# Optimization experiments

Hardware: AMD Instinct MI355X
Metric: run time of the kernel (lower is better)

The kernel has to match this reference:

```python
import jax, jax.numpy as jnp
import numpy as np

B, T, D, H, G = 32, 1000, 512, 512, 8
LN_EPS = 1e-5


def setup_inputs() -> dict:
    key = jax.random.key(0)
    ks = jax.random.split(key, 6)
    return {
        "x": jax.random.normal(ks[0], (B, T, D), jnp.float32),
        "w_in": jax.random.normal(ks[1], (G, D // G, H // G), jnp.float32) * 0.05,
        "w_rec_W": jax.random.normal(ks[2], (2 * H, H), jnp.float32) * 0.05,
        "u_rec": jax.random.normal(ks[3], (2 * H, H), jnp.float32) * 0.05,
        "ln_gamma": jnp.ones((2 * H,), jnp.float32),
        "ln_beta": jnp.zeros((2 * H,), jnp.float32),
        "w_out": jax.random.normal(ks[4], (G, H // G, D // G), jnp.float32) * 0.05,
    }


def grouped_linear(x, w):
    # x: [B,T,G*I], w: [G,I,Ho] -> [B,T,G*Ho]
    b, t, _ = x.shape
    g, i, ho = w.shape
    y = jnp.einsum('btgi,gih->btgh', x.reshape(b, t, g, i), w)
    return y.reshape(b, t, g * ho)


def layernorm(w, gamma, beta):
    mu = jnp.mean(w, axis=-1, keepdims=True)
    var = jnp.var(w, axis=-1, keepdims=True)
    return (w - mu) * jax.lax.rsqrt(var + LN_EPS) * gamma + beta


def ligru_scan(w, u):
    # w: [B,T,2H] precomputed input projection; u: [2H,H] recurrent weight
    ut = u.T  # [H, 2H]
    h0 = jnp.zeros((w.shape[0], u.shape[1]), w.dtype)

    def step(h, wt):
        gates = wt + h @ ut            # [B, 2H]
        at, zt = jnp.split(gates, 2, axis=1)
        zt = jax.nn.sigmoid(zt)
        hcand = jax.nn.relu(at)        # drop_mask = 1.0 (eval)
        h = zt * h + (1.0 - zt) * hcand
        return h, h

    _, hs = jax.lax.scan(step, h0, jnp.swapaxes(w, 0, 1))  # [T,B,H]
    return jnp.swapaxes(hs, 0, 1)  # [B,T,H]


def reference(x, w_in, w_rec_W, u_rec, ln_gamma, ln_beta, w_out):
    h_in = grouped_linear(x, w_in)              # [B,T,H]
    w = jnp.einsum('bth,gh->btg', h_in, w_rec_W)  # [B,T,2H]
    w = layernorm(w, ln_gamma, ln_beta)
    h = ligru_scan(w, u_rec)                    # [B,T,H]
    return grouped_linear(h, w_out)             # [B,T,D]
```

## Files before the change

### kernel.cpp

```cpp
#include <hip/hip_runtime.h>
#include <cstddef>

#define B_SZ 32
#define T_LEN 1000
#define LN_EPS 1e-5f

typedef short bf16x8 __attribute__((ext_vector_type(8)));
typedef float f32x4 __attribute__((ext_vector_type(4)));

__device__ __forceinline__ unsigned short f2bf(float f) {
    unsigned u = __builtin_bit_cast(unsigned, f);
    u += 0x7FFFu + ((u >> 16) & 1u);
    return (unsigned short)(u >> 16);
}

__global__ __launch_bounds__(256) void kw(const float* __restrict__ w_rec,
                                          unsigned short* __restrict__ wrt) {
    int idx  = blockIdx.x * 256 + threadIdx.x;
    int lane = idx & 63;
    int nt   = (idx >> 6) & 63;
    int kt   = idx >> 12;
    int n    = nt * 16 + (lane & 15);
    int k0   = kt * 32 + (lane >> 4) * 8;
    const float* src = w_rec + (size_t)n * 512 + k0;
    unsigned short* dst = wrt + (size_t)idx * 8;
#pragma unroll
    for (int j = 0; j < 8; ++j) dst[j] = f2bf(src[j]);
}

__global__ __launch_bounds__(256) void k1(const float* __restrict__ x,
                                          const float* __restrict__ w_in,
                                          unsigned short* __restrict__ hin) {
    __shared__ alignas(16) float xt[16][512];
    const int tid  = threadIdx.x;
    const int row0 = blockIdx.x * 16;

    for (int i = tid; i < 16 * 128; i += 256) {
        int rr = i >> 7, c4 = i & 127;
        ((float4*)xt[rr])[c4] =
            ((const float4*)(x + (size_t)(row0 + rr) * 512))[c4];
    }
    __syncthreads();

    for (int q = 0; q < 2; ++q) {
        const int c = tid + (q << 8);
        const int g = c >> 6, o = c & 63;
        const float* wb = w_in + (g << 12) + o;
        float wcol[64];
#pragma unroll
        for (int ii = 0; ii < 64; ++ii) wcol[ii] = wb[ii << 6];
#pragma unroll 4
        for (int rr = 0; rr < 16; ++rr) {
            float acc = 0.f;
#pragma unroll
            for (int ii = 0; ii < 64; ++ii) acc += xt[rr][(g << 6) + ii] * wcol[ii];
            hin[(size_t)(row0 + rr) * 512 + c] = f2bf(acc);
        }
    }
}

#define ALD 536
__global__ __launch_bounds__(256) void k2(const unsigned short* __restrict__ hin,
                                          const unsigned short* __restrict__ wrt,
                                          const float* __restrict__ gamma,
                                          const float* __restrict__ beta,
                                          float* __restrict__ w_pre) {
    __shared__ alignas(16) unsigned short At[32 * ALD];
    __shared__ float redS[4][32];
    __shared__ float redQ[4][32];
    __shared__ float stat[2][32];

    const int tid  = threadIdx.x;
    const int w    = tid >> 6;
    const int l    = tid & 63;
    const int kgrp = l >> 4;
    const int lc   = l & 15;
    const int row0 = blockIdx.x * 32;

    for (int sidx = tid; sidx < 2048; sidx += 256) {
        int r = sidx >> 6, sg = sidx & 63;
        *(bf16x8*)(At + r * ALD + sg * 8) =
            *(const bf16x8*)(hin + (size_t)(row0 + r) * 512 + sg * 8);
    }
    __syncthreads();

    f32x4 acc[2][16];
#pragma unroll
    for (int fr = 0; fr < 2; ++fr)
#pragma unroll
        for (int n = 0; n < 16; ++n) acc[fr][n] = f32x4{0.f, 0.f, 0.f, 0.f};

    for (int kt = 0; kt < 16; ++kt) {
        bf16x8 a0 = *(const bf16x8*)(At + (lc)      * ALD + kt * 32 + kgrp * 8);
        bf16x8 a1 = *(const bf16x8*)(At + (16 + lc) * ALD + kt * 32 + kgrp * 8);
        const unsigned short* bb =
            wrt + (((size_t)kt * 64 + w * 16) * 64 + l) * 8;
#pragma unroll
        for (int ntl = 0; ntl < 16; ++ntl) {
            bf16x8 bf = *(const bf16x8*)(bb + (size_t)ntl * 512);
            acc[0][ntl] = __builtin_amdgcn_mfma_f32_16x16x32_bf16(a0, bf, acc[0][ntl], 0, 0, 0);
            acc[1][ntl] = __builtin_amdgcn_mfma_f32_16x16x32_bf16(a1, bf, acc[1][ntl], 0, 0, 0);
        }
    }

    float sums[2][4] = {{0.f}}, sqs[2][4] = {{0.f}};
#pragma unroll
    for (int fr = 0; fr < 2; ++fr)
#pragma unroll
        for (int ntl = 0; ntl < 16; ++ntl)
#pragma unroll
            for (int r = 0; r < 4; ++r) {
                float v = acc[fr][ntl][r];
                sums[fr][r] += v;
                sqs[fr][r]  += v * v;
            }
#pragma unroll
    for (int off = 1; off < 16; off <<= 1)
#pragma unroll
        for (int fr = 0; fr < 2; ++fr)
#pragma unroll
            for (int r = 0; r < 4; ++r) {
                sums[fr][r] += __shfl_xor(sums[fr][r], off);
                sqs[fr][r]  += __shfl_xor(sqs[fr][r], off);
            }
    if (lc == 0) {
#pragma unroll
        for (int fr = 0; fr < 2; ++fr)
#pragma unroll
            for (int r = 0; r < 4; ++r) {
                redS[w][fr * 16 + kgrp * 4 + r] = sums[fr][r];
                redQ[w][fr * 16 + kgrp * 4 + r] = sqs[fr][r];
            }
    }
    __syncthreads();
    if (tid < 32) {
        float S = redS[0][tid] + redS[1][tid] + redS[2][tid] + redS[3][tid];
        float Q = redQ[0][tid] + redQ[1][tid] + redQ[2][tid] + redQ[3][tid];
        float mu  = S * (1.f / 1024.f);
        float var = Q * (1.f / 1024.f) - mu * mu;
        stat[0][tid] = mu;
        stat[1][tid] = rsqrtf(var + LN_EPS);
    }
    __syncthreads();

#pragma unroll
    for (int ntl = 0; ntl < 16; ++ntl) {
        const int col = (w << 8) + (ntl << 4) + lc;
        const float g = gamma[col], bt = beta[col];
#pragma unroll
        for (int fr = 0; fr < 2; ++fr)
#pragma unroll
            for (int r = 0; r < 4; ++r) {
                const int row = fr * 16 + kgrp * 4 + r;
                const float mu  = stat[0][row];
                const float inv = stat[1][row];
                w_pre[((size_t)(row0 + row) << 10) + col] =
                    (acc[fr][ntl][r] - mu) * inv * g + bt;
            }
    }
}

__global__ __launch_bounds__(1024) void k_scan(const float* __restrict__ w_pre,
                                               const float* __restrict__ u,
                                               float* __restrict__ hs,
                                               unsigned int* hbuf) {
    __shared__ alignas(16) float hsh[512];
    __shared__ float gsum[128];

    const int tid = threadIdx.x;
    const int b   = blockIdx.x & 31;
    const int s   = blockIdx.x >> 5;
    const int J0  = s << 6;
    const int row = tid >> 3;
    const int kk  = tid & 7;
    const int jj  = (row < 64) ? (J0 + row) : (448 + J0 + row);

    float ur[64];
    {
        const float4* up = (const float4*)(u + (size_t)jj * 512 + (kk << 6));
#pragma unroll
        for (int m = 0; m < 16; ++m) {
            float4 v = up[m];
            ur[4 * m + 0] = v.x; ur[4 * m + 1] = v.y;
            ur[4 * m + 2] = v.z; ur[4 * m + 3] = v.w;
        }
    }

    const float* wbase = w_pre + ((size_t)b * T_LEN) * 1024 + jj;
    float* outbase = hs + ((size_t)b * T_LEN) * 512 + J0;
    const char* hb8 = (const char*)hsh;

    float hreg = 0.f;

    for (int t = 0; t < T_LEN; ++t) {
        unsigned int* in_w  = hbuf + ((((t & 1) << 5) | b) << 9);
        unsigned int* out_w = hbuf + (((((t + 1) & 1) << 5) | b) << 9);

        float wreg = 0.f;
        if (kk == 0) wreg = wbase[(size_t)t << 10];

        if (tid < 512) {
            const unsigned int want = (unsigned)t & 3u;
            unsigned int v = __hip_atomic_load(in_w + tid, __ATOMIC_RELAXED,
                                               __HIP_MEMORY_SCOPE_AGENT);
            while ((v & 3u) != want) {
                v = __hip_atomic_load(in_w + tid, __ATOMIC_RELAXED,
                                      __HIP_MEMORY_SCOPE_AGENT);
            }
            float hv = __builtin_bit_cast(float, v);
            int c = tid >> 2, r = tid & 3;
            int a = (c & ~7) | ((c ^ (c >> 4)) & 7);
            hsh[(a << 2) | r] = hv;
        }
        __syncthreads();

        float a0 = 0.f, a1 = 0.f, a2 = 0.f, a3 = 0.f;
        const int base = kk << 8;
#pragma unroll
        for (int i = 0; i < 16; ++i) {
            int off = base + (((i & 8) | ((i ^ kk) & 7)) << 4);
            float4 hv = *(const float4*)(hb8 + off);
            a0 += ur[4 * i + 0] * hv.x;
            a1 += ur[4 * i + 1] * hv.y;
            a2 += ur[4 * i + 2] * hv.z;
            a3 += ur[4 * i + 3] * hv.w;
        }
        float acc = (a0 + a1) + (a2 + a3);
        acc += __shfl_xor(acc, 1);
        acc += __shfl_xor(acc, 2);
        acc += __shfl_xor(acc, 4);
        if (kk == 0) gsum[row] = acc + wreg;
        __syncthreads();

        if (tid < 64) {
            float a  = gsum[tid];
            float zl = gsum[64 + tid];
            float z  = 1.f / (1.f + __expf(-zl));
            float hn = z * hreg + (1.f - z) * fmaxf(a, 0.f);
            hreg = hn;
            unsigned int bits = (__builtin_bit_cast(unsigned int, hn) & ~3u) |
                                ((unsigned)(t + 1) & 3u);
            __hip_atomic_store(out_w + J0 + tid, bits, __ATOMIC_RELAXED,
                               __HIP_MEMORY_SCOPE_AGENT);
            outbase[((size_t)t << 9) + tid] = hn;
        }
    }
}

__global__ __launch_bounds__(256) void k_out(const float* __restrict__ w_out,
                                             float* __restrict__ io) {
    __shared__ alignas(16) float ht[8][512];
    const int tid  = threadIdx.x;
    const int row0 = blockIdx.x * 8;

    for (int i = tid; i < 8 * 128; i += 256) {
        int rr = i >> 7, c4 = i & 127;
        ((float4*)ht[rr])[c4] =
            ((const float4*)(io + (size_t)(row0 + rr) * 512))[c4];
    }
    __syncthreads();

    for (int q = 0; q < 2; ++q) {
        const int c = tid + (q << 8);
        const int g = c >> 6, o = c & 63;
        const float* wb = w_out + (g << 12) + o;
        float wcol[64];
#pragma unroll
        for (int ii = 0; ii < 64; ++ii) wcol[ii] = wb[ii << 6];
#pragma unroll 4
        for (int rr = 0; rr < 8; ++rr) {
            float acc = 0.f;
#pragma unroll
            for (int ii = 0; ii < 64; ++ii) acc += ht[rr][(g << 6) + ii] * wcol[ii];
            io[(size_t)(row0 + rr) * 512 + c] = acc;
        }
    }
}

extern "C" void kernel_launch(void* const* d_in, const int* in_sizes, int n_in,
                              void* d_out, int out_size, void* d_ws, size_t ws_size,
                              hipStream_t stream) {
    const float* x      = (const float*)d_in[0];
    const float* w_in   = (const float*)d_in[1];
    const float* w_rec  = (const float*)d_in[2];
    const float* u_rec  = (const float*)d_in[3];
    const float* gamma  = (const float*)d_in[4];
    const float* beta   = (const float*)d_in[5];
    const float* w_out  = (const float*)d_in[6];
    float* out = (float*)d_out;

    float*        w_pre = (float*)d_ws;
    unsigned int* hbuf  = (unsigned int*)(w_pre + (size_t)32 * T_LEN * 1024);

    unsigned short* hin = (unsigned short*)d_out;
    unsigned short* wrt = hin + (size_t)32000 * 512;

    hipLaunchKernelGGL(kw, dim3(256), dim3(256), 0, stream, w_rec, wrt);
    hipLaunchKernelGGL(k1, dim3(2000), dim3(256), 0, stream, x, w_in, hin);
    hipLaunchKernelGGL(k2, dim3(1000), dim3(256), 0, stream,
                       hin, wrt, gamma, beta, w_pre);
    hipMemsetAsync(hbuf, 0, 2 * 32 * 512 * sizeof(unsigned int), stream);
    hipLaunchKernelGGL(k_scan, dim3(256), dim3(1024), 0, stream,
                       w_pre, u_rec, out, hbuf);
    hipLaunchKernelGGL(k_out, dim3(4000), dim3(256), 0, stream, w_out, out);
}
```

Measured before the change: 1.844 ms.

## Interleave gate rows per wave to drop second barrier in LiGRU scan step

The recurrent scan kernel now interleaves the a and z rows of each hidden unit, so adjacent 8-lane groups hold both gates. The gate combination happens in registers through a shuffle instead of a shared-memory gsum array followed by a second __syncthreads. The h-state shared buffer is double-buffered so the next step's writes cannot race with this step's reads. Polling of the cross-block h exchange uses 64-bit loads with half as many threads, and one lane per wave publishes four values. This shortens the per-timestep serial critical path, at the cost of redundant gate math across lanes and more complex stamp checking.

```diff
diff --git a/kernel.cpp b/kernel.cpp
--- a/kernel.cpp
+++ b/kernel.cpp
@@ -164,8 +164,7 @@
                                                const float* __restrict__ u,
                                                float* __restrict__ hs,
                                                unsigned int* hbuf) {
-    __shared__ alignas(16) float hsh[512];
-    __shared__ float gsum[128];
+    __shared__ alignas(16) float hsh[2][512];
 
     const int tid = threadIdx.x;
     const int b   = blockIdx.x & 31;
@@ -173,7 +172,8 @@
     const int J0  = s << 6;
     const int row = tid >> 3;
     const int kk  = tid & 7;
-    const int jj  = (row < 64) ? (J0 + row) : (448 + J0 + row);
+    const int jh  = row >> 1;
+    const int jj  = (row & 1) ? (512 + J0 + jh) : (J0 + jh);
 
     float ur[64];
     {
@@ -187,8 +187,9 @@
     }
 
     const float* wbase = w_pre + ((size_t)b * T_LEN) * 1024 + jj;
-    float* outbase = hs + ((size_t)b * T_LEN) * 512 + J0;
-    const char* hb8 = (const char*)hsh;
+    const int wv = tid >> 6;
+    const int ln = tid & 63;
+    float* outrow = hs + ((size_t)b * T_LEN) * 512 + J0 + (wv << 2);
 
     float hreg = 0.f;
 
@@ -199,21 +200,23 @@
         float wreg = 0.f;
         if (kk == 0) wreg = wbase[(size_t)t << 10];
 
-        if (tid < 512) {
+        if (tid < 256) {
+            const unsigned long long* src = (const unsigned long long*)in_w + tid;
             const unsigned int want = (unsigned)t & 3u;
-            unsigned int v = __hip_atomic_load(in_w + tid, __ATOMIC_RELAXED,
-                                               __HIP_MEMORY_SCOPE_AGENT);
-            while ((v & 3u) != want) {
-                v = __hip_atomic_load(in_w + tid, __ATOMIC_RELAXED,
+            unsigned long long v = __hip_atomic_load(src, __ATOMIC_RELAXED,
+                                                     __HIP_MEMORY_SCOPE_AGENT);
+            while (((unsigned)v & 3u) != want ||
+                   ((unsigned)(v >> 32) & 3u) != want) {
+                v = __hip_atomic_load(src, __ATOMIC_RELAXED,
                                       __HIP_MEMORY_SCOPE_AGENT);
             }
-            float hv = __builtin_bit_cast(float, v);
-            int c = tid >> 2, r = tid & 3;
+            int c = tid >> 1, half = tid & 1;
             int a = (c & ~7) | ((c ^ (c >> 4)) & 7);
-            hsh[(a << 2) | r] = hv;
+            *(unsigned long long*)((char*)hsh[t & 1] + (a << 4) + (half << 3)) = v;
         }
         __syncthreads();
 
+        const char* hb8 = (const char*)hsh[t & 1];
         float a0 = 0.f, a1 = 0.f, a2 = 0.f, a3 = 0.f;
         const int base = kk << 8;
 #pragma unroll
@@ -225,24 +228,32 @@
             a2 += ur[4 * i + 2] * hv.z;
             a3 += ur[4 * i + 3] * hv.w;
         }
-        float acc = (a0 + a1) + (a2 + a3);
+        float acc = (a0 + a1) + (a2 + a3) + wreg;
         acc += __shfl_xor(acc, 1);
         acc += __shfl_xor(acc, 2);
         acc += __shfl_xor(acc, 4);
-        if (kk == 0) gsum[row] = acc + wreg;
-        __syncthreads();
-
-        if (tid < 64) {
-            float a  = gsum[tid];
-            float zl = gsum[64 + tid];
-            float z  = 1.f / (1.f + __expf(-zl));
-            float hn = z * hreg + (1.f - z) * fmaxf(a, 0.f);
-            hreg = hn;
-            unsigned int bits = (__builtin_bit_cast(unsigned int, hn) & ~3u) |
-                                ((unsigned)(t + 1) & 3u);
-            __hip_atomic_store(out_w + J0 + tid, bits, __ATOMIC_RELAXED,
-                               __HIP_MEMORY_SCOPE_AGENT);
-            outbase[((size_t)t << 9) + tid] = hn;
+        float other = __shfl_xor(acc, 8);
+        float ga = (row & 1) ? other : acc;
+        float gz = (row & 1) ? acc : other;
+        float z  = 1.f / (1.f + __expf(-gz));
+        float hn = z * hreg + (1.f - z) * fmaxf(ga, 0.f);
+        hreg = hn;
+
+        float h1 = __shfl(hn, 16, 64);
+        float h2 = __shfl(hn, 32, 64);
+        float h3 = __shfl(hn, 48, 64);
+        if (ln == 0) {
+            const unsigned int stamp = (unsigned)(t + 1) & 3u;
+            unsigned int b0 = (__builtin_bit_cast(unsigned int, hn) & ~3u) | stamp;
+            unsigned int b1 = (__builtin_bit_cast(unsigned int, h1) & ~3u) | stamp;
+            unsigned int b2 = (__builtin_bit_cast(unsigned int, h2) & ~3u) | stamp;
+            unsigned int b3 = (__builtin_bit_cast(unsigned int, h3) & ~3u) | stamp;
+            unsigned int* dst = out_w + J0 + (wv << 2);
+            __hip_atomic_store(dst + 0, b0, __ATOMIC_RELAXED, __HIP_MEMORY_SCOPE_AGENT);
+            __hip_atomic_store(dst + 1, b1, __ATOMIC_RELAXED, __HIP_MEMORY_SCOPE_AGENT);
+            __hip_atomic_store(dst + 2, b2, __ATOMIC_RELAXED, __HIP_MEMORY_SCOPE_AGENT);
+            __hip_atomic_store(dst + 3, b3, __ATOMIC_RELAXED, __HIP_MEMORY_SCOPE_AGENT);
+            *(float4*)(outrow + ((size_t)t << 9)) = float4{hn, h1, h2, h3};
         }
     }
 }
```

Result: slower. 5.754 ms (+212.0%).
